# Kernel optimization log

Hardware: AMD Instinct MI355X
Metric: run time of the kernel (lower is better)

Reference implementation:

```python
import jax, jax.numpy as jnp
import numpy as np


def setup_inputs() -> dict:
    key = jax.random.key(0)
    k1, k2 = jax.random.split(key)
    x = jax.random.normal(k1, (16, 4096, 3), dtype=jnp.float32)  # [B, N, 3]
    y = jax.random.normal(k2, (16, 4096, 3), dtype=jnp.float32)  # [B, M, 3]
    return {"x": x, "y": y}


def reference(x, y):
    # Squared pairwise distances via the ||x||^2 + ||y||^2 - 2<x,y> expansion.
    # d: [B, N, M]
    x2 = jnp.sum(x * x, axis=-1)  # [B, N]
    y2 = jnp.sum(y * y, axis=-1)  # [B, M]
    xy = jnp.einsum('bnd,bmd->bnm', x, y)  # [B, N, M]
    d = x2[:, :, None] + y2[:, None, :] - 2.0 * xy
    # directed Chamfer terms: mean over own points of min sq-dist to other cloud
    dist_to_y = jnp.mean(jnp.min(d, axis=2), axis=1)  # [B] (x -> y)
    dist_to_x = jnp.mean(jnp.min(d, axis=1), axis=1)  # [B] (y -> x)
    # per-cloud max of the two directed distances, averaged over batch
    return jnp.mean(jnp.maximum(dist_to_y, dist_to_x))
```

## Files before the change

### kernel.cpp

```cpp
#include <hip/hip_runtime.h>


typedef __attribute__((ext_vector_type(8)))  short bf16x8;
typedef __attribute__((ext_vector_type(16))) float f32x16;

#define BATCH   16
#define NPTS    4096
#define DB      (2 * BATCH)
#define GM_F32  (2 * DB * NPTS)

static __device__ __forceinline__ unsigned bf16rn(float f) {
  unsigned u = __float_as_uint(f);
  return (u + 0x7FFFu + ((u >> 16) & 1u)) >> 16;
}
static __device__ __forceinline__ float bf2f(unsigned h) {
  return __uint_as_float(h << 16);
}
static __device__ __forceinline__ unsigned pk(unsigned lo, unsigned hi) {
  return (lo & 0xFFFFu) | (hi << 16);
}

__global__ __launch_bounds__(512, 4) void chamfer_mm(
    const float* __restrict__ x, const float* __restrict__ y,
    float* __restrict__ gm, unsigned* __restrict__ cnt) {
  __shared__ __align__(16) uint4 afl[64 * 64];

  const int bid = blockIdx.x;
  const int tid = threadIdx.x;
  if (bid == 0 && tid == 0) *cnt = 0;

  const int db  = bid >> 4;
  const int r   = bid & 15;
  const int c   = r >> 1;
  const int h   = r & 1;
  const int dir = db >> 4, b = db & 15;
  const float* own   = (dir == 0 ? x : y) + (size_t)b * NPTS * 3;
  const float* other = (dir == 0 ? y : x) + (size_t)b * NPTS * 3;
  const float* mp    = other + (size_t)h * 2048 * 3;

  #pragma unroll
  for (int k = 0; k < 4; ++k) {
    const int p = tid + k * 512;
    float y0 = mp[p * 3 + 0], y1 = mp[p * 3 + 1], y2 = mp[p * 3 + 2];
    float wv = fmaf(y2, y2, fmaf(y1, y1, y0 * y0));
    float z0 = -2.f * y0, z1 = -2.f * y1, z2 = -2.f * y2;
    unsigned h0 = bf16rn(z0), h1 = bf16rn(z1), h2 = bf16rn(z2);
    unsigned e0 = bf16rn(z0 - bf2f(h0));
    unsigned e1 = bf16rn(z1 - bf2f(h1));
    unsigned e2 = bf16rn(z2 - bf2f(h2));
    unsigned wh = bf16rn(wv), wl = bf16rn(wv - bf2f(wh));
    const int tile = p >> 5, row = p & 31;
    afl[tile * 64 + row]      =
        make_uint4(pk(h0, h1), pk(h2, e0), pk(e1, e2), pk(h0, h1));
    afl[tile * 64 + 32 + row] =
        make_uint4(pk(h2, wh), pk(wl, 0u), 0u, 0u);
  }

  const int w = tid >> 6, l = tid & 63;
  const int col = l & 31, kh = l >> 5;
  const unsigned ONE = 0x3F80u;
  bf16x8 bfr[2];
  float sq[2], rmn[2];
  #pragma unroll
  for (int nt = 0; nt < 2; ++nt) {
    const int n = c * 512 + w * 64 + nt * 32 + col;
    float a0 = own[n * 3 + 0], a1 = own[n * 3 + 1], a2 = own[n * 3 + 2];
    sq[nt]  = fmaf(a2, a2, fmaf(a1, a1, a0 * a0));
    rmn[nt] = 1e30f;
    unsigned h0 = bf16rn(a0), h1 = bf16rn(a1), h2 = bf16rn(a2);
    unsigned e0 = bf16rn(a0 - bf2f(h0));
    unsigned e1 = bf16rn(a1 - bf2f(h1));
    unsigned e2 = bf16rn(a2 - bf2f(h2));
    union { unsigned uu[4]; bf16x8 v; } U;
    U.uu[0] = (kh == 0) ? pk(h0, h1) : pk(e2, ONE);
    U.uu[1] = (kh == 0) ? pk(h2, h0) : pk(ONE, 0u);
    U.uu[2] = (kh == 0) ? pk(h1, h2) : 0u;
    U.uu[3] = (kh == 0) ? pk(e0, e1) : 0u;
    bfr[nt] = U.v;
  }
  __syncthreads();

  const int aoff = kh * 32 + col;
  const f32x16 z16 = {0.f, 0.f, 0.f, 0.f, 0.f, 0.f, 0.f, 0.f,
                      0.f, 0.f, 0.f, 0.f, 0.f, 0.f, 0.f, 0.f};
  #pragma unroll 4
  for (int mt = 0; mt < 64; ++mt) {
    union { uint4 u; bf16x8 v; } A;
    A.u = afl[mt * 64 + aoff];
    #pragma unroll
    for (int nt = 0; nt < 2; ++nt) {
      f32x16 acc = __builtin_amdgcn_mfma_f32_32x32x16_bf16(
          A.v, bfr[nt], z16, 0, 0, 0);
      float m0 = fminf(fminf(acc[0],  acc[1]),  acc[2]);
      float m1 = fminf(fminf(acc[3],  acc[4]),  acc[5]);
      float m2 = fminf(fminf(acc[6],  acc[7]),  acc[8]);
      float m3 = fminf(fminf(acc[9],  acc[10]), acc[11]);
      float m4 = fminf(fminf(acc[12], acc[13]), acc[14]);
      float m5 = fminf(fminf(acc[15], m0), m1);
      float m6 = fminf(fminf(m2, m3), m4);
      rmn[nt] = fminf(fminf(m5, m6), rmn[nt]);
    }
  }

  #pragma unroll
  for (int nt = 0; nt < 2; ++nt) {
    float v = fminf(rmn[nt], __shfl_xor(rmn[nt], 32, 64));
    float sv = v + sq[nt];
    if (l < 32)
      gm[(size_t)(h * DB + db) * NPTS + c * 512 + w * 64 + nt * 32 + col] = sv;
  }
}

__global__ __launch_bounds__(256) void chamfer_combine(
    const float* __restrict__ gm, float* __restrict__ dist,
    unsigned* __restrict__ cnt, float* __restrict__ out) {
  const int db = blockIdx.x;
  const float* g0 = gm + (size_t)db * NPTS;
  const float* g1 = gm + (size_t)(DB + db) * NPTS;
  float s = 0.0f;
  for (int i = threadIdx.x; i < NPTS; i += 256)
    s += fminf(g0[i], g1[i]);
  #pragma unroll
  for (int off = 32; off > 0; off >>= 1) s += __shfl_down(s, off, 64);
  __shared__ float red[4];
  const int lane = threadIdx.x & 63, wid = threadIdx.x >> 6;
  if (lane == 0) red[wid] = s;
  __syncthreads();
  if (threadIdx.x == 0) {
    dist[db] = ((red[0] + red[1]) + (red[2] + red[3])) * (1.0f / (float)NPTS);
    __threadfence();
    unsigned old = __hip_atomic_fetch_add(cnt, 1u, __ATOMIC_ACQ_REL,
                                          __HIP_MEMORY_SCOPE_AGENT);
    if (old == DB - 1) {
      __threadfence();
      float acc = 0.0f;
      #pragma unroll
      for (int b = 0; b < BATCH; ++b) {
        float d0 = __uint_as_float(__hip_atomic_load(
            (const unsigned*)&dist[b], __ATOMIC_RELAXED,
            __HIP_MEMORY_SCOPE_AGENT));
        float d1 = __uint_as_float(__hip_atomic_load(
            (const unsigned*)&dist[b + BATCH], __ATOMIC_RELAXED,
            __HIP_MEMORY_SCOPE_AGENT));
        acc += fmaxf(d0, d1);
      }
      out[0] = acc * (1.0f / (float)BATCH);
    }
  }
}

extern "C" void kernel_launch(void* const* d_in, const int* in_sizes, int n_in,
                              void* d_out, int out_size, void* d_ws, size_t ws_size,
                              hipStream_t stream) {
  const float* x = (const float*)d_in[0];
  const float* y = (const float*)d_in[1];
  float* out = (float*)d_out;

  float* gm     = (float*)d_ws;
  float* dist   = gm + GM_F32;
  unsigned* cnt = (unsigned*)(dist + DB);

  chamfer_mm<<<512, 512, 0, stream>>>(x, y, gm, cnt);
  chamfer_combine<<<DB, 256, 0, stream>>>(gm, dist, cnt, out);
}
```

Measured before the change: 29.81 us.

## Fuse combine into main kernel with full-M staged loop per block

```diff
diff --git a/kernel.cpp b/kernel.cpp
--- a/kernel.cpp
+++ b/kernel.cpp
@@ -7,7 +7,10 @@
 #define BATCH   16
 #define NPTS    4096
 #define DB      (2 * BATCH)
-#define GM_F32  (2 * DB * NPTS)
+#define TPB     256
+#define CHUNK   128
+#define NBLK    (DB * (NPTS / CHUNK))
+#define NSTAGE  4
 
 static __device__ __forceinline__ unsigned bf16rn(float f) {
   unsigned u = __float_as_uint(f);
@@ -20,53 +23,31 @@
   return (lo & 0xFFFFu) | (hi << 16);
 }
 
-__global__ __launch_bounds__(512, 4) void chamfer_mm(
+__global__ __launch_bounds__(TPB, 4) void chamfer_mm(
     const float* __restrict__ x, const float* __restrict__ y,
-    float* __restrict__ gm, unsigned* __restrict__ cnt) {
-  __shared__ __align__(16) uint4 afl[64 * 64];
+    float* __restrict__ partials, unsigned* __restrict__ cnt,
+    float* __restrict__ out) {
+  __shared__ __align__(16) uint4 afl[32 * 64];
+  __shared__ float red[4];
+  __shared__ int isLast;
 
   const int bid = blockIdx.x;
   const int tid = threadIdx.x;
-  if (bid == 0 && tid == 0) *cnt = 0;
-
-  const int db  = bid >> 4;
-  const int r   = bid & 15;
-  const int c   = r >> 1;
-  const int h   = r & 1;
+  const int db  = bid >> 5;
+  const int c   = bid & 31;
   const int dir = db >> 4, b = db & 15;
   const float* own   = (dir == 0 ? x : y) + (size_t)b * NPTS * 3;
   const float* other = (dir == 0 ? y : x) + (size_t)b * NPTS * 3;
-  const float* mp    = other + (size_t)h * 2048 * 3;
-
-  #pragma unroll
-  for (int k = 0; k < 4; ++k) {
-    const int p = tid + k * 512;
-    float y0 = mp[p * 3 + 0], y1 = mp[p * 3 + 1], y2 = mp[p * 3 + 2];
-    float wv = fmaf(y2, y2, fmaf(y1, y1, y0 * y0));
-    float z0 = -2.f * y0, z1 = -2.f * y1, z2 = -2.f * y2;
-    unsigned h0 = bf16rn(z0), h1 = bf16rn(z1), h2 = bf16rn(z2);
-    unsigned e0 = bf16rn(z0 - bf2f(h0));
-    unsigned e1 = bf16rn(z1 - bf2f(h1));
-    unsigned e2 = bf16rn(z2 - bf2f(h2));
-    unsigned wh = bf16rn(wv), wl = bf16rn(wv - bf2f(wh));
-    const int tile = p >> 5, row = p & 31;
-    afl[tile * 64 + row]      =
-        make_uint4(pk(h0, h1), pk(h2, e0), pk(e1, e2), pk(h0, h1));
-    afl[tile * 64 + 32 + row] =
-        make_uint4(pk(h2, wh), pk(wl, 0u), 0u, 0u);
-  }
 
   const int w = tid >> 6, l = tid & 63;
   const int col = l & 31, kh = l >> 5;
   const unsigned ONE = 0x3F80u;
-  bf16x8 bfr[2];
-  float sq[2], rmn[2];
-  #pragma unroll
-  for (int nt = 0; nt < 2; ++nt) {
-    const int n = c * 512 + w * 64 + nt * 32 + col;
+  bf16x8 bfr;
+  float sq;
+  {
+    const int n = c * CHUNK + w * 32 + col;
     float a0 = own[n * 3 + 0], a1 = own[n * 3 + 1], a2 = own[n * 3 + 2];
-    sq[nt]  = fmaf(a2, a2, fmaf(a1, a1, a0 * a0));
-    rmn[nt] = 1e30f;
+    sq = fmaf(a2, a2, fmaf(a1, a1, a0 * a0));
     unsigned h0 = bf16rn(a0), h1 = bf16rn(a1), h2 = bf16rn(a2);
     unsigned e0 = bf16rn(a0 - bf2f(h0));
     unsigned e1 = bf16rn(a1 - bf2f(h1));
@@ -76,75 +57,93 @@
     U.uu[1] = (kh == 0) ? pk(h2, h0) : pk(ONE, 0u);
     U.uu[2] = (kh == 0) ? pk(h1, h2) : 0u;
     U.uu[3] = (kh == 0) ? pk(e0, e1) : 0u;
-    bfr[nt] = U.v;
+    bfr = U.v;
   }
-  __syncthreads();
 
   const int aoff = kh * 32 + col;
   const f32x16 z16 = {0.f, 0.f, 0.f, 0.f, 0.f, 0.f, 0.f, 0.f,
                       0.f, 0.f, 0.f, 0.f, 0.f, 0.f, 0.f, 0.f};
-  #pragma unroll 4
-  for (int mt = 0; mt < 64; ++mt) {
-    union { uint4 u; bf16x8 v; } A;
-    A.u = afl[mt * 64 + aoff];
+  float rm[8];
+  #pragma unroll
+  for (int j = 0; j < 8; ++j) rm[j] = 1e30f;
+
+  for (int st = 0; st < NSTAGE; ++st) {
+    __syncthreads();
+    const float* mp = other + (size_t)st * 1024 * 3;
     #pragma unroll
-    for (int nt = 0; nt < 2; ++nt) {
+    for (int k = 0; k < 4; ++k) {
+      const int p = tid + k * TPB;
+      float y0 = mp[p * 3 + 0], y1 = mp[p * 3 + 1], y2 = mp[p * 3 + 2];
+      float wv = fmaf(y2, y2, fmaf(y1, y1, y0 * y0));
+      float z0 = -2.f * y0, z1 = -2.f * y1, z2 = -2.f * y2;
+      unsigned h0 = bf16rn(z0), h1 = bf16rn(z1), h2 = bf16rn(z2);
+      unsigned e0 = bf16rn(z0 - bf2f(h0));
+      unsigned e1 = bf16rn(z1 - bf2f(h1));
+      unsigned e2 = bf16rn(z2 - bf2f(h2));
+      unsigned wh = bf16rn(wv), wl = bf16rn(wv - bf2f(wh));
+      const int tile = p >> 5, row = p & 31;
+      afl[tile * 64 + row]      =
+          make_uint4(pk(h0, h1), pk(h2, e0), pk(e1, e2), pk(h0, h1));
+      afl[tile * 64 + 32 + row] =
+          make_uint4(pk(h2, wh), pk(wl, 0u), 0u, 0u);
+    }
+    __syncthreads();
+
+    #pragma unroll 4
+    for (int mt = 0; mt < 32; ++mt) {
+      union { uint4 u; bf16x8 v; } A;
+      A.u = afl[mt * 64 + aoff];
       f32x16 acc = __builtin_amdgcn_mfma_f32_32x32x16_bf16(
-          A.v, bfr[nt], z16, 0, 0, 0);
-      float m0 = fminf(fminf(acc[0],  acc[1]),  acc[2]);
-      float m1 = fminf(fminf(acc[3],  acc[4]),  acc[5]);
-      float m2 = fminf(fminf(acc[6],  acc[7]),  acc[8]);
-      float m3 = fminf(fminf(acc[9],  acc[10]), acc[11]);
-      float m4 = fminf(fminf(acc[12], acc[13]), acc[14]);
-      float m5 = fminf(fminf(acc[15], m0), m1);
-      float m6 = fminf(fminf(m2, m3), m4);
-      rmn[nt] = fminf(fminf(m5, m6), rmn[nt]);
+          A.v, bfr, z16, 0, 0, 0);
+      #pragma unroll
+      for (int j = 0; j < 8; ++j)
+        rm[j] = fminf(fminf(acc[2 * j], acc[2 * j + 1]), rm[j]);
     }
   }
 
+  float v;
+  {
+    float t0 = fminf(fminf(rm[0], rm[1]), rm[2]);
+    float t1 = fminf(fminf(rm[3], rm[4]), rm[5]);
+    float t2 = fminf(rm[6], rm[7]);
+    v = fminf(fminf(t0, t1), t2);
+    v = fminf(v, __shfl_xor(v, 32, 64));
+    v += sq;
+  }
   #pragma unroll
-  for (int nt = 0; nt < 2; ++nt) {
-    float v = fminf(rmn[nt], __shfl_xor(rmn[nt], 32, 64));
-    float sv = v + sq[nt];
-    if (l < 32)
-      gm[(size_t)(h * DB + db) * NPTS + c * 512 + w * 64 + nt * 32 + col] = sv;
-  }
-}
+  for (int m = 1; m <= 16; m <<= 1) v += __shfl_xor(v, m, 64);
+  if (l == 0) red[w] = v;
+  __syncthreads();
+  if (tid == 0)
+    partials[bid] = (red[0] + red[1]) + (red[2] + red[3]);
 
-__global__ __launch_bounds__(256) void chamfer_combine(
-    const float* __restrict__ gm, float* __restrict__ dist,
-    unsigned* __restrict__ cnt, float* __restrict__ out) {
-  const int db = blockIdx.x;
-  const float* g0 = gm + (size_t)db * NPTS;
-  const float* g1 = gm + (size_t)(DB + db) * NPTS;
-  float s = 0.0f;
-  for (int i = threadIdx.x; i < NPTS; i += 256)
-    s += fminf(g0[i], g1[i]);
-  #pragma unroll
-  for (int off = 32; off > 0; off >>= 1) s += __shfl_down(s, off, 64);
-  __shared__ float red[4];
-  const int lane = threadIdx.x & 63, wid = threadIdx.x >> 6;
-  if (lane == 0) red[wid] = s;
-  __syncthreads();
-  if (threadIdx.x == 0) {
-    dist[db] = ((red[0] + red[1]) + (red[2] + red[3])) * (1.0f / (float)NPTS);
+  if (tid == 0) {
     __threadfence();
     unsigned old = __hip_atomic_fetch_add(cnt, 1u, __ATOMIC_ACQ_REL,
                                           __HIP_MEMORY_SCOPE_AGENT);
-    if (old == DB - 1) {
-      __threadfence();
-      float acc = 0.0f;
+    isLast = (old == NBLK - 1);
+  }
+  __syncthreads();
+  if (isLast) {
+    __threadfence();
+    float* dls = (float*)afl;
+    if (tid < DB) {
+      float s = 0.0f;
+      #pragma unroll 8
+      for (int j = 0; j < 32; ++j) {
+        unsigned uv = __hip_atomic_load(
+            (const unsigned*)&partials[tid * 32 + j], __ATOMIC_RELAXED,
+            __HIP_MEMORY_SCOPE_AGENT);
+        s += __uint_as_float(uv);
+      }
+      dls[tid] = s * (1.0f / (float)NPTS);
+    }
+    __syncthreads();
+    if (tid < BATCH) {
+      float mx = fmaxf(dls[tid], dls[tid + BATCH]);
       #pragma unroll
-      for (int b = 0; b < BATCH; ++b) {
-        float d0 = __uint_as_float(__hip_atomic_load(
-            (const unsigned*)&dist[b], __ATOMIC_RELAXED,
-            __HIP_MEMORY_SCOPE_AGENT));
-        float d1 = __uint_as_float(__hip_atomic_load(
-            (const unsigned*)&dist[b + BATCH], __ATOMIC_RELAXED,
-            __HIP_MEMORY_SCOPE_AGENT));
-        acc += fmaxf(d0, d1);
-      }
-      out[0] = acc * (1.0f / (float)BATCH);
+      for (int off = 8; off > 0; off >>= 1) mx += __shfl_down(mx, off, 16);
+      if (tid == 0) out[0] = mx * (1.0f / (float)BATCH);
     }
   }
 }
@@ -156,10 +155,9 @@
   const float* y = (const float*)d_in[1];
   float* out = (float*)d_out;
 
-  float* gm     = (float*)d_ws;
-  float* dist   = gm + GM_F32;
-  unsigned* cnt = (unsigned*)(dist + DB);
+  float* partials = (float*)d_ws;
+  unsigned* cnt   = (unsigned*)(partials + NBLK);
 
-  chamfer_mm<<<512, 512, 0, stream>>>(x, y, gm, cnt);
-  chamfer_combine<<<DB, 256, 0, stream>>>(gm, dist, cnt, out);
+  hipMemsetAsync(cnt, 0, 4, stream);
+  chamfer_mm<<<NBLK, TPB, 0, stream>>>(x, y, partials, cnt, out);
 }
```

After: 55.66 us. 86.7% more time.
